# Performance work log

Measured on AMD Instinct MI355X. Metric: run time of the kernel, lower is better.

The kernel has to match this reference:

```python
import jax, jax.numpy as jnp
import numpy as np

K = 50          # NEC paper uses p=50 neighbors
DELTA = 1e-3    # kernel smoothing constant


def setup_inputs() -> dict:
    key = jax.random.key(0)
    ks = jax.random.split(key, 8)
    B, D_IN, D, A, C = 512, 2, 128, 3, 200000
    s = lambda fan_in: 1.0 / np.sqrt(fan_in)
    return {
        "x": jax.random.normal(ks[0], (B, D_IN), jnp.float32),
        "W1": jax.random.normal(ks[1], (D_IN, D), jnp.float32) * s(D_IN),
        "b1": jnp.zeros((D,), jnp.float32),
        "W2": jax.random.normal(ks[2], (D, D), jnp.float32) * s(D),
        "b2": jnp.zeros((D,), jnp.float32),
        "W3": jax.random.normal(ks[3], (D, D), jnp.float32) * s(D),
        "b3": jnp.zeros((D,), jnp.float32),
        "W4": jax.random.normal(ks[4], (D, D), jnp.float32) * s(D),
        "b4": jnp.zeros((D,), jnp.float32),
        "keys": jax.random.normal(ks[5], (A, C, D), jnp.float32),
        "mem_values": jax.random.normal(ks[6], (A, C), jnp.float32),
    }


def _encode(x, W1, b1, W2, b2, W3, b3, W4, b4):
    h = jax.nn.relu(x @ W1 + b1)
    h = jax.nn.relu(h @ W2 + b2)
    h = jax.nn.relu(h @ W3 + b3)
    return h @ W4 + b4  # [B, D]


def _dnd_lookup(h, keys, mem_values):
    # h: [B, D]; keys: [A, C, D]; mem_values: [A, C]
    q2 = jnp.sum(h * h, axis=-1)                       # [B]
    k2 = jnp.sum(keys * keys, axis=-1)                 # [A, C]
    cross = jnp.einsum("bd,acd->bac", h, keys)         # [B, A, C]
    d2 = jnp.maximum(q2[:, None, None] + k2[None] - 2.0 * cross, 0.0)
    neg_d, idx = jax.lax.top_k(-d2, K)                  # [B, A, K]
    d_top = -neg_d
    w = 1.0 / (d_top + DELTA)                           # NEC kernel
    w = w / jnp.sum(w, axis=-1, keepdims=True)
    a_idx = jnp.arange(keys.shape[0])[None, :, None]    # [1, A, 1]
    v_top = mem_values[a_idx, idx]                      # gather -> [B, A, K]
    values = jnp.sum(w * v_top, axis=-1)                # [B, A]
    return values


def reference(x, W1, b1, W2, b2, W3, b3, W4, b4, keys, mem_values):
    h = _encode(x, W1, b1, W2, b2, W3, b3, W4, b4)
    values = _dnd_lookup(h, keys, mem_values)
    actions = jnp.argmax(values, axis=-1)
    return values, actions
```

## Files before the change

kernel.cpp:

```cpp
#include <hip/hip_runtime.h>
#include <hip/hip_bf16.h>
#include <math.h>

#define B_    512
#define DIM   128
#define A_    3
#define C_    200000
#define K_    50
#define DELTA 1e-3

typedef __attribute__((ext_vector_type(8))) short bf16x8;
typedef __attribute__((ext_vector_type(4))) float f32x4;

#define NBIN_A 128
#define CAP_A  1024
#define NSEG_G 128
#define TPS_G  13
#define NT_G   1563
#define HSEG   16
#define CHPS   782
#define ROWCH  12500

#define AOFF_H64   0u
#define AOFF_H32   524288u
#define AOFF_HBF   786432u
#define AOFF_Q2    917504u
#define AOFF_HIST  919552u
#define AOFF_CNT   1705984u
#define AOFF_TAUB  1712128u
#define AOFF_V64   1718272u
#define AOFF_CAND  1730560u
#define AOFF_BINS  8022016u
#define NEED_A     (8022016ull + 307200000ull)

#define NBIN_B 192
#define CAP_B  768
#define BM_B   64
#define BN_B   128
#define TPC_B  16
#define CHUNK_B (TPC_B*BN_B)
#define NCH_B  ((C_ + CHUNK_B - 1)/CHUNK_B)

#define BOFF_H32   0u
#define BOFF_H64   262144u
#define BOFF_Q2    786432u
#define BOFF_K2    788480u
#define BOFF_HIST  3188480u
#define BOFF_TAU   4368128u
#define BOFF_CNT   4374272u
#define BOFF_V64   4380416u
#define BOFF_CAND  4392704u

static __device__ inline unsigned short f2bf(float x) {
    union { float f; unsigned u; } c; c.f = x;
    unsigned r = (c.u + 0x7FFFu + ((c.u >> 16) & 1u)) >> 16;
    return (unsigned short)r;
}
static __device__ inline unsigned pkbf(float a, float b) {
    __hip_bfloat162 t = __float22bfloat162_rn(make_float2(a, b));
    union { __hip_bfloat162 h; unsigned u; } cv; cv.h = t; return cv.u;
}

__global__ __launch_bounds__(128) void mlp_kernel(
    const float* __restrict__ x,
    const float* __restrict__ W1, const float* __restrict__ b1,
    const float* __restrict__ W2, const float* __restrict__ b2,
    const float* __restrict__ W3, const float* __restrict__ b3,
    const float* __restrict__ W4, const float* __restrict__ b4,
    float* __restrict__ h32, unsigned short* __restrict__ hbf,
    double* __restrict__ h64, float* __restrict__ q2)
{
    int b = blockIdx.x, t = threadIdx.x;
    __shared__ double s0[DIM], s1[DIM];
    double x0 = (double)x[b*2+0], x1 = (double)x[b*2+1];
    double h = x0*(double)W1[t] + x1*(double)W1[DIM+t] + (double)b1[t];
    s0[t] = h > 0.0 ? h : 0.0;
    __syncthreads();
    double acc = (double)b2[t];
    for (int k = 0; k < DIM; k++) acc += s0[k]*(double)W2[k*DIM+t];
    s1[t] = acc > 0.0 ? acc : 0.0;
    __syncthreads();
    acc = (double)b3[t];
    for (int k = 0; k < DIM; k++) acc += s1[k]*(double)W3[k*DIM+t];
    s0[t] = acc > 0.0 ? acc : 0.0;
    __syncthreads();
    acc = (double)b4[t];
    for (int k = 0; k < DIM; k++) acc += s0[k]*(double)W4[k*DIM+t];
    h64[b*DIM+t] = acc;
    float hf = (float)acc;
    h32[b*DIM+t] = hf;
    hbf[b*DIM+t] = f2bf(hf);
    s1[t] = acc*acc;
    __syncthreads();
    for (int s = 64; s > 0; s >>= 1) { if (t < s) s1[t] += s1[t+s]; __syncthreads(); }
    if (t == 0) q2[b] = (float)s1[0];
}

__global__ __launch_bounds__(512, 4) void gemm_bin_kernel(
    const float* __restrict__ keys, const unsigned short* __restrict__ hbf,
    const float* __restrict__ q2, unsigned char* __restrict__ bins)
{
    const int seg = blockIdx.x, my = blockIdx.y, a = blockIdx.z;
    const int b0 = my*128;
    const int tid = threadIdx.x;
    const int lane = tid & 63, w = tid >> 6;
    const int lm = lane & 15, kh = lane >> 4;
    const int wn = w & 3, wm = w >> 2;

    int tc = NT_G - seg*TPS_G;
    if (tc <= 0) return;
    if (tc > TPS_G) tc = TPS_G;

    __shared__ short sA[128*136];
    __shared__ short sB[128*136];
    __shared__ float q2s[128];
    __shared__ float k2s[128];

    const int r = tid >> 2, hh = tid & 3;

    {
        const int4* gp = (const int4*)hbf + (size_t)(b0 + r)*16 + hh*4;
        int4* dp = (int4*)&sA[r*136 + hh*32];
        #pragma unroll
        for (int q = 0; q < 4; q++) dp[q] = gp[q];
        if (tid < 128) q2s[tid] = q2[b0 + tid];
    }

    for (int t = 0; t < tc; t++) {
        int n0 = (seg*TPS_G + t)*128;
        __syncthreads();

        {
            int nr = n0 + r; if (nr >= C_) nr = C_-1;
            const float4* gp = (const float4*)(keys + ((size_t)a*C_ + nr)*128) + hh*8;
            float ss = 0.0f;
            int4* dp = (int4*)&sB[r*136 + hh*32];
            #pragma unroll
            for (int q = 0; q < 4; q++) {
                float4 v0 = gp[2*q], v1 = gp[2*q+1];
                ss += v0.x*v0.x + v0.y*v0.y + v0.z*v0.z + v0.w*v0.w
                    + v1.x*v1.x + v1.y*v1.y + v1.z*v1.z + v1.w*v1.w;
                int4 pk;
                pk.x = (int)pkbf(v0.x, v0.y);
                pk.y = (int)pkbf(v0.z, v0.w);
                pk.z = (int)pkbf(v1.x, v1.y);
                pk.w = (int)pkbf(v1.z, v1.w);
                dp[q] = pk;
            }
            ss += __shfl_xor(ss, 1, 64);
            ss += __shfl_xor(ss, 2, 64);
            if (hh == 0) k2s[r] = ss;
        }
        __syncthreads();

        f32x4 acc[2][4];
        #pragma unroll
        for (int i = 0; i < 2; i++)
            #pragma unroll
            for (int j = 0; j < 4; j++) acc[i][j] = (f32x4){0.f, 0.f, 0.f, 0.f};

        #pragma unroll
        for (int kst = 0; kst < 4; kst++) {
            bf16x8 af[2], bfv[4];
            #pragma unroll
            for (int i = 0; i < 2; i++)
                af[i] = *(const bf16x8*)&sB[(wn*32 + i*16 + lm)*136 + kst*32 + kh*8];
            #pragma unroll
            for (int j = 0; j < 4; j++)
                bfv[j] = *(const bf16x8*)&sA[(wm*64 + j*16 + lm)*136 + kst*32 + kh*8];
            #pragma unroll
            for (int i = 0; i < 2; i++)
                #pragma unroll
                for (int j = 0; j < 4; j++)
                    acc[i][j] = __builtin_amdgcn_mfma_f32_16x16x32_bf16(af[i], bfv[j], acc[i][j], 0, 0, 0);
        }

        unsigned char* bp = bins + ((size_t)(a*B_ + b0))*C_ + n0;
        #pragma unroll
        for (int i = 0; i < 2; i++) {
            int nl = wn*32 + i*16 + kh*4;
            int n = n0 + nl;
            if (n < C_) {
                float4 kq = *(const float4*)&k2s[nl];
                #pragma unroll
                for (int j = 0; j < 4; j++) {
                    int bcol = wm*64 + j*16 + lm;
                    float q2v = q2s[bcol];
                    unsigned pk = 0;
                    #pragma unroll
                    for (int rg = 0; rg < 4; rg++) {
                        float kv = (rg == 0) ? kq.x : (rg == 1) ? kq.y : (rg == 2) ? kq.z : kq.w;
                        float d2v = (q2v + kv) - 2.0f*acc[i][j][rg];
                        float dc = fminf(fmaxf(d2v, 16.0f), 4095.0f);
                        unsigned bin = (__float_as_uint(dc) >> 19) - 2096u;
                        pk |= bin << (8*rg);
                    }
                    *(unsigned*)(bp + (size_t)bcol*C_ + nl) = pk;
                }
            }
        }
    }
}

__global__ __launch_bounds__(256) void histA_kernel(const unsigned char* __restrict__ bins,
                                                    unsigned* __restrict__ hist)
{
    int q = blockIdx.x;
    int seg = blockIdx.y;
    int tid = threadIdx.x;
    int a = q >> 9, b = q & 511;
    int p = b*A_ + a;
    __shared__ unsigned hs[NBIN_A*8];
    for (int i = tid; i < NBIN_A*8; i += 256) hs[i] = 0;
    __syncthreads();
    const uint4* row = (const uint4*)(bins + (size_t)q*C_);
    int ch0 = seg*CHPS, ch1 = ch0 + CHPS; if (ch1 > ROWCH) ch1 = ROWCH;
    int rep = tid & 7;
    for (int ch = ch0 + tid; ch < ch1; ch += 256) {
        uint4 v = row[ch];
        unsigned d[4] = {v.x, v.y, v.z, v.w};
        #pragma unroll
        for (int e = 0; e < 4; e++) {
            unsigned x = d[e];
            atomicAdd(&hs[((x      ) & 127u)*8 + rep], 1u);
            atomicAdd(&hs[((x >>  8) & 127u)*8 + rep], 1u);
            atomicAdd(&hs[((x >> 16) & 127u)*8 + rep], 1u);
            atomicAdd(&hs[((x >> 24) & 127u)*8 + rep], 1u);
        }
    }
    __syncthreads();
    if (tid < NBIN_A) {
        unsigned s = 0;
        #pragma unroll
        for (int r2 = 0; r2 < 8; r2++) s += hs[tid*8 + r2];
        if (s) atomicAdd(&hist[(size_t)p*NBIN_A + tid], s);
    }
}

__global__ void tauA_kernel(const unsigned* __restrict__ hist, int* __restrict__ taubin)
{
    int p = blockIdx.x*256 + threadIdx.x;
    if (p >= B_*A_) return;
    const unsigned* hp = hist + (size_t)p*NBIN_A;
    unsigned cum = 0; int jsel = NBIN_A-1;
    for (int j = 0; j < NBIN_A; j++) { cum += hp[j]; if (cum >= K_) { jsel = j; break; } }
    unsigned c1 = cum + (jsel+1 < NBIN_A ? hp[jsel+1] : 0u);
    unsigned c2 = c1  + (jsel+2 < NBIN_A ? hp[jsel+2] : 0u);
    int jt = (c2 <= 768u) ? jsel+2 : jsel+1;
    if (jt > NBIN_A-1) jt = NBIN_A-1;
    taubin[p] = jt;
}

__global__ __launch_bounds__(256) void collectA_kernel(const unsigned char* __restrict__ bins,
    const int* __restrict__ taubin, unsigned* __restrict__ cnt, int* __restrict__ cand)
{
    int q = blockIdx.x, seg = blockIdx.y, tid = threadIdx.x;
    int a = q >> 9, b = q & 511;
    int p = b*A_ + a;
    int tb = taubin[p];
    unsigned thr  = (unsigned)(tb + 1);
    unsigned addv = (128u - thr) * 0x01010101u;
    const uint4* row = (const uint4*)(bins + (size_t)q*C_);
    int ch0 = seg*CHPS, ch1 = ch0 + CHPS; if (ch1 > ROWCH) ch1 = ROWCH;
    for (int ch = ch0 + tid; ch < ch1; ch += 256) {
        uint4 v = row[ch];
        unsigned d[4] = {v.x, v.y, v.z, v.w};
        #pragma unroll
        for (int e = 0; e < 4; e++) {
            unsigned m = (d[e] + addv) & 0x80808080u;
            if (m != 0x80808080u) {
                #pragma unroll
                for (int by = 0; by < 4; by++) {
                    if (!((m >> (8*by + 7)) & 1u)) {
                        int n = ch*16 + e*4 + by;
                        unsigned pos = atomicAdd(&cnt[p], 1u);
                        if (pos < CAP_A) cand[(size_t)p*CAP_A + pos] = n;
                    }
                }
            }
        }
    }
}

__global__ __launch_bounds__(256) void k2_kernel(const float* __restrict__ keys,
                                                 float* __restrict__ k2)
{
    int r = blockIdx.x*4 + (threadIdx.x >> 6);
    int lane = threadIdx.x & 63;
    float2 v = ((const float2*)keys)[(size_t)r*64 + lane];
    float s = v.x*v.x + v.y*v.y;
    #pragma unroll
    for (int off = 32; off > 0; off >>= 1) s += __shfl_down(s, off, 64);
    if (lane == 0) k2[r] = s;
}

template<int MODE>
__global__ __launch_bounds__(256) void pass_kernel(
    const float* __restrict__ keys, const float* __restrict__ h32,
    const float* __restrict__ q2,   const float* __restrict__ k2,
    unsigned* __restrict__ hist,    const float* __restrict__ tau,
    unsigned* __restrict__ cnt,     int* __restrict__ cand)
{
    const int bt = blockIdx.x;
    const int ch = blockIdx.y;
    const int a  = blockIdx.z;
    const int b0 = bt*BM_B;
    const int tid = threadIdx.x;
    const int tx = tid & 31, ty = tid >> 5;

    __shared__ float4 hs4[BM_B*33];
    __shared__ float4 ks4[BN_B*33];
    __shared__ float  q2s[BM_B];
    __shared__ float  taus[BM_B];
    __shared__ unsigned hist_s[MODE == 0 ? BM_B*NBIN_B : 1];

    #pragma unroll
    for (int q = 0; q < BM_B*32/256; q++) {
        int flat = q*256 + tid; int row = flat >> 5, kq = flat & 31;
        hs4[row*33 + kq] = ((const float4*)h32)[(size_t)(b0+row)*32 + kq];
    }
    if (tid < BM_B) {
        q2s[tid] = q2[b0+tid];
        if (MODE == 1) taus[tid] = tau[(b0+tid)*A_ + a];
    }
    if (MODE == 0) for (int i = tid; i < BM_B*NBIN_B; i += 256) hist_s[i] = 0;
    const float* __restrict__ k2g = k2 + (size_t)a*C_;

    for (int t = 0; t < TPC_B; t++) {
        int n0 = ch*CHUNK_B + t*BN_B;
        if (n0 >= C_) break;
        __syncthreads();
        #pragma unroll
        for (int q = 0; q < 16; q++) {
            int flat = q*256 + tid; int row = flat >> 5, kq = flat & 31;
            int nr = n0 + row; if (nr >= C_) nr = C_-1;
            ks4[row*33 + kq] = ((const float4*)keys)[((size_t)a*C_ + nr)*32 + kq];
        }
        __syncthreads();

        float acc[8][4];
        #pragma unroll
        for (int i = 0; i < 8; i++)
            #pragma unroll
            for (int j = 0; j < 4; j++) acc[i][j] = 0.0f;

        for (int kq = 0; kq < 32; kq++) {
            float4 hv[8], kv[4];
            #pragma unroll
            for (int i = 0; i < 8; i++) hv[i] = hs4[(ty*8+i)*33 + kq];
            #pragma unroll
            for (int j = 0; j < 4; j++) kv[j] = ks4[(j*32+tx)*33 + kq];
            #pragma unroll
            for (int i = 0; i < 8; i++)
                #pragma unroll
                for (int j = 0; j < 4; j++)
                    acc[i][j] += hv[i].x*kv[j].x + hv[i].y*kv[j].y
                               + hv[i].z*kv[j].z + hv[i].w*kv[j].w;
        }

        #pragma unroll
        for (int i = 0; i < 8; i++) {
            int bl = ty*8 + i;
            float q2b = q2s[bl];
            #pragma unroll
            for (int j = 0; j < 4; j++) {
                int n = n0 + j*32 + tx;
                if (n < C_) {
                    float d2f = fmaxf(q2b + k2g[n] - 2.0f*acc[i][j], 0.0f);
                    if (MODE == 0) {
                        int bin = (int)(__float_as_uint(d2f + 1.0f) >> 19) - 2032;
                        bin = bin < 0 ? 0 : (bin > NBIN_B-1 ? NBIN_B-1 : bin);
                        atomicAdd(&hist_s[bl*NBIN_B + bin], 1u);
                    } else {
                        if (d2f < taus[bl]) {
                            int p = (b0+bl)*A_ + a;
                            unsigned pos = atomicAdd(&cnt[p], 1u);
                            if (pos < CAP_B) cand[(size_t)p*CAP_B + pos] = n;
                        }
                    }
                }
            }
        }
    }
    if (MODE == 0) {
        __syncthreads();
        for (int i = tid; i < BM_B*NBIN_B; i += 256) {
            unsigned v = hist_s[i];
            if (v) {
                int bl = i / NBIN_B, bin = i % NBIN_B;
                atomicAdd(&hist[(size_t)((b0+bl)*A_ + a)*NBIN_B + bin], v);
            }
        }
    }
}

__global__ __launch_bounds__(256) void tauB_kernel(const unsigned* __restrict__ hist,
                                                   float* __restrict__ tau)
{
    int p = blockIdx.x*256 + threadIdx.x;
    if (p >= B_*A_) return;
    const unsigned* hp = hist + (size_t)p*NBIN_B;
    unsigned cum = 0; int jsel = NBIN_B-1;
    for (int j = 0; j < NBIN_B; j++) { cum += hp[j]; if (cum >= K_) { jsel = j; break; } }
    tau[p] = __uint_as_float((unsigned)(2034 + jsel) << 19) - 1.0f;
}

__global__ __launch_bounds__(256) void select_kernel(
    const float* __restrict__ keys, const double* __restrict__ h64,
    const float* __restrict__ mem_values,
    const unsigned* __restrict__ cnt, const int* __restrict__ cand,
    float* __restrict__ out_values, double* __restrict__ val64, int cap)
{
    int p = blockIdx.x; int b = p / A_, a = p % A_;
    int tid = threadIdx.x;
    __shared__ double hd[DIM];
    __shared__ double d2s[CAP_A];
    __shared__ float  vs[CAP_A];
    __shared__ double redv[4];
    __shared__ int    redi4[4];
    __shared__ double acc_w, acc_wv;

    for (int i = tid; i < DIM; i += 256) hd[i] = h64[(size_t)b*DIM + i];
    if (tid == 0) { acc_w = 0.0; acc_wv = 0.0; }
    __syncthreads();

    int n = (int)cnt[p]; if (n > cap) n = cap;
    for (int i = tid; i < n; i += 256) {
        int c = cand[(size_t)p*cap + i];
        const float4* kr = (const float4*)(keys + ((size_t)a*C_ + c)*DIM);
        double s0 = 0.0, s1 = 0.0;
        #pragma unroll 4
        for (int kq = 0; kq < 32; kq++) {
            float4 kv = kr[kq];
            double d0 = hd[4*kq+0] - (double)kv.x;
            double d1 = hd[4*kq+1] - (double)kv.y;
            double d2 = hd[4*kq+2] - (double)kv.z;
            double d3 = hd[4*kq+3] - (double)kv.w;
            s0 += d0*d0 + d1*d1; s1 += d2*d2 + d3*d3;
        }
        d2s[i] = s0 + s1;
        vs[i]  = mem_values[(size_t)a*C_ + c];
    }
    __syncthreads();

    int kk = n < K_ ? n : K_;
    for (int t = 0; t < kk; t++) {
        double best = 1e300; int bi = -1;
        for (int i = tid; i < n; i += 256)
            if (d2s[i] < best) { best = d2s[i]; bi = i; }
        #pragma unroll
        for (int off = 32; off > 0; off >>= 1) {
            double ov = __shfl_xor(best, off, 64);
            int    oi = __shfl_xor(bi,   off, 64);
            if (ov < best) { best = ov; bi = oi; }
        }
        int wv = tid >> 6;
        if ((tid & 63) == 0) { redv[wv] = best; redi4[wv] = bi; }
        __syncthreads();
        if (tid == 0) {
            double bv = redv[0]; int wi = redi4[0];
            if (redv[1] < bv) { bv = redv[1]; wi = redi4[1]; }
            if (redv[2] < bv) { bv = redv[2]; wi = redi4[2]; }
            if (redv[3] < bv) { bv = redv[3]; wi = redi4[3]; }
            double d = d2s[wi]; if (d < 0.0) d = 0.0;
            double wgt = 1.0 / (d + DELTA);
            acc_w += wgt; acc_wv += wgt * (double)vs[wi];
            d2s[wi] = 2e300;
        }
        __syncthreads();
    }
    if (tid == 0) {
        double v = acc_wv / acc_w;
        out_values[p] = (float)v;
        val64[p] = v;
    }
}

__global__ void argmax_kernel(const double* __restrict__ val64, float* __restrict__ out)
{
    int b = blockIdx.x*blockDim.x + threadIdx.x;
    if (b >= B_) return;
    double v0 = val64[b*A_+0], v1 = val64[b*A_+1], v2 = val64[b*A_+2];
    int bi = 0; double bv = v0;
    if (v1 > bv) { bv = v1; bi = 1; }
    if (v2 > bv) { bv = v2; bi = 2; }
    out[B_*A_ + b] = (float)bi;
}

extern "C" void kernel_launch(void* const* d_in, const int* in_sizes, int n_in,
                              void* d_out, int out_size, void* d_ws, size_t ws_size,
                              hipStream_t stream)
{
    const float* x    = (const float*)d_in[0];
    const float* W1   = (const float*)d_in[1];
    const float* b1   = (const float*)d_in[2];
    const float* W2   = (const float*)d_in[3];
    const float* b2   = (const float*)d_in[4];
    const float* W3   = (const float*)d_in[5];
    const float* b3   = (const float*)d_in[6];
    const float* W4   = (const float*)d_in[7];
    const float* b4   = (const float*)d_in[8];
    const float* keys = (const float*)d_in[9];
    const float* memv = (const float*)d_in[10];

    char* ws = (char*)d_ws;

    if (ws_size >= NEED_A) {
        double*         h64  = (double*)        (ws + AOFF_H64);
        float*          h32  = (float*)         (ws + AOFF_H32);
        unsigned short* hbf  = (unsigned short*)(ws + AOFF_HBF);
        float*          q2   = (float*)         (ws + AOFF_Q2);
        unsigned*       hist = (unsigned*)      (ws + AOFF_HIST);
        unsigned*       cnt  = (unsigned*)      (ws + AOFF_CNT);
        int*            taub = (int*)           (ws + AOFF_TAUB);
        double*         v64  = (double*)        (ws + AOFF_V64);
        int*            cand = (int*)           (ws + AOFF_CAND);
        unsigned char*  bins = (unsigned char*) (ws + AOFF_BINS);

        hipMemsetAsync(ws + AOFF_HIST, 0, (AOFF_CNT + B_*A_*4) - AOFF_HIST, stream);

        mlp_kernel<<<B_, 128, 0, stream>>>(x, W1, b1, W2, b2, W3, b3, W4, b4, h32, hbf, h64, q2);
        gemm_bin_kernel<<<dim3(NSEG_G, 4, A_), 512, 0, stream>>>(keys, hbf, q2, bins);
        histA_kernel<<<dim3(B_*A_, HSEG), 256, 0, stream>>>(bins, hist);
        tauA_kernel<<<(B_*A_ + 255)/256, 256, 0, stream>>>(hist, taub);
        collectA_kernel<<<dim3(B_*A_, HSEG), 256, 0, stream>>>(bins, taub, cnt, cand);
        select_kernel<<<B_*A_, 256, 0, stream>>>(keys, h64, memv, cnt, cand, (float*)d_out, v64, CAP_A);
        argmax_kernel<<<2, 256, 0, stream>>>(v64, (float*)d_out);
    } else {
        float*          h32  = (float*)         (ws + BOFF_H32);
        double*         h64  = (double*)        (ws + BOFF_H64);
        float*          q2   = (float*)         (ws + BOFF_Q2);
        float*          k2   = (float*)         (ws + BOFF_K2);
        unsigned*       hist = (unsigned*)      (ws + BOFF_HIST);
        float*          tau  = (float*)         (ws + BOFF_TAU);
        unsigned*       cnt  = (unsigned*)      (ws + BOFF_CNT);
        double*         v64  = (double*)        (ws + BOFF_V64);
        int*            cand = (int*)           (ws + BOFF_CAND);
        unsigned short* hbf  = (unsigned short*)(ws + BOFF_CAND);

        hipMemsetAsync(ws + BOFF_HIST, 0, (BOFF_CNT + B_*A_*4) - BOFF_HIST, stream);

        mlp_kernel<<<B_, 128, 0, stream>>>(x, W1, b1, W2, b2, W3, b3, W4, b4, h32, hbf, h64, q2);
        k2_kernel<<<(A_*C_)/4, 256, 0, stream>>>(keys, k2);
        pass_kernel<0><<<dim3(B_/BM_B, NCH_B, A_), 256, 0, stream>>>(keys, h32, q2, k2, hist, nullptr, nullptr, nullptr);
        tauB_kernel<<<(B_*A_ + 255)/256, 256, 0, stream>>>(hist, tau);
        pass_kernel<1><<<dim3(B_/BM_B, NCH_B, A_), 256, 0, stream>>>(keys, h32, q2, k2, nullptr, tau, cnt, cand);
        select_kernel<<<B_*A_, 256, 0, stream>>>(keys, h64, memv, cnt, cand, (float*)d_out, v64, CAP_B);
        argmax_kernel<<<2, 256, 0, stream>>>(v64, (float*)d_out);
    }
}
```

Baseline: 1.105 ms.

## Pre-convert keys to swizzled bf16 and double-buffer GEMM with direct-to-LDS loads

Adds a conversion pass that writes keys once as bf16 in an XOR-swizzled layout, together with precomputed key norms. A new GEMM kernel then streams these bf16 tiles into LDS with global_load_lds, double-buffered, instead of having each of the 4 row blocks re-read and re-convert the fp32 keys. The intent is to cut repeated fp32 key traffic and conversion work in the GEMM and to overlap loads with MFMA. The cost is an extra kernel with a full key read plus a bf16 write, a larger workspace requirement, and a path that falls back to the old kernel when the workspace is too small.

```diff
diff --git a/kernel.cpp b/kernel.cpp
--- a/kernel.cpp
+++ b/kernel.cpp
@@ -33,6 +33,14 @@
 #define AOFF_BINS  8022016u
 #define NEED_A     (8022016ull + 307200000ull)
 
+#define NSEG2  125
+#define TPS2   25
+#define NT2    3125
+#define KBF_ASTR 51200000ull
+#define AOFF_KBF 315222016ull
+#define AOFF_K2A (AOFF_KBF + 3ull*KBF_ASTR)
+#define NEED_A2  (AOFF_K2A + 2400000ull)
+
 #define NBIN_B 192
 #define CAP_B  768
 #define BM_B   64
@@ -61,6 +69,12 @@
     union { __hip_bfloat162 h; unsigned u; } cv; cv.h = t; return cv.u;
 }
 
+static __device__ inline void gl_lds16(const void* g, void* l) {
+    __builtin_amdgcn_global_load_lds(
+        (const __attribute__((address_space(1))) void*)g,
+        (__attribute__((address_space(3))) void*)l, 16, 0, 0);
+}
+
 __global__ __launch_bounds__(128) void mlp_kernel(
     const float* __restrict__ x,
     const float* __restrict__ W1, const float* __restrict__ b1,
@@ -96,6 +110,134 @@
     if (t == 0) q2[b] = (float)s1[0];
 }
 
+__global__ __launch_bounds__(256) void conv_kernel(
+    const float* __restrict__ keys, unsigned char* __restrict__ kbf,
+    float* __restrict__ k2a)
+{
+    int bid = blockIdx.x;
+    int a = bid / 12500;
+    int base = (bid - a*12500)*256 + threadIdx.x;
+    int n = base >> 4, cc = base & 15;
+    const float4* gp = (const float4*)(keys + ((size_t)a*C_ + n)*128 + cc*8);
+    float4 v0 = gp[0], v1 = gp[1];
+    float ss = v0.x*v0.x + v0.y*v0.y + v0.z*v0.z + v0.w*v0.w
+             + v1.x*v1.x + v1.y*v1.y + v1.z*v1.z + v1.w*v1.w;
+    int4 pk;
+    pk.x = (int)pkbf(v0.x, v0.y);
+    pk.y = (int)pkbf(v0.z, v0.w);
+    pk.z = (int)pkbf(v1.x, v1.y);
+    pk.w = (int)pkbf(v1.z, v1.w);
+    *(int4*)(kbf + (size_t)a*KBF_ASTR + (size_t)n*256 + ((cc ^ (n & 7)) << 4)) = pk;
+    ss += __shfl_xor(ss, 1, 64);
+    ss += __shfl_xor(ss, 2, 64);
+    ss += __shfl_xor(ss, 4, 64);
+    ss += __shfl_xor(ss, 8, 64);
+    if (cc == 0) k2a[(size_t)a*C_ + n] = ss;
+}
+
+__global__ __launch_bounds__(512, 4) void gemm2_kernel(
+    const unsigned char* __restrict__ kbf, const unsigned short* __restrict__ hbf,
+    const float* __restrict__ q2, const float* __restrict__ k2a,
+    unsigned char* __restrict__ bins)
+{
+    const int seg = blockIdx.x, my = blockIdx.y, a = blockIdx.z;
+    const int b0 = my*128;
+    const int tid = threadIdx.x;
+    const int lane = tid & 63, w = tid >> 6;
+    const int lm = lane & 15, kh = lane >> 4;
+    const int wn = w & 1, wm = w >> 1;
+
+    __shared__ short sA[16384];
+    __shared__ short sB[2][8192];
+    __shared__ float q2s[128];
+
+    {
+        int r = tid >> 2, hh = tid & 3;
+        const int4* gp = (const int4*)hbf + (size_t)(b0 + r)*16 + hh*4;
+        #pragma unroll
+        for (int q = 0; q < 4; q++) {
+            int cc = hh*4 + q;
+            *(int4*)((char*)sA + r*256 + ((cc ^ (r & 7)) << 4)) = gp[q];
+        }
+        if (tid < 128) q2s[tid] = q2[b0 + tid];
+    }
+
+    const unsigned char* kbfa = kbf + (size_t)a*KBF_ASTR;
+    const float* __restrict__ k2g = k2a + (size_t)a*C_;
+    const int t0 = seg*TPS2;
+
+    {
+        const char* src = (const char*)kbfa + (size_t)t0*16384 + tid*16;
+        char* dst = (char*)&sB[0][0] + w*1024;
+        gl_lds16(src, dst);
+        gl_lds16(src + 8192, dst + 8192);
+    }
+    __syncthreads();
+
+    int cur = 0;
+    for (int t = 0; t < TPS2; t++) {
+        int n0 = (t0 + t)*64;
+
+        if (t + 1 < TPS2) {
+            const char* src = (const char*)kbfa + (size_t)(t0 + t + 1)*16384 + tid*16;
+            char* dst = (char*)&sB[cur ^ 1][0] + w*1024;
+            gl_lds16(src, dst);
+            gl_lds16(src + 8192, dst + 8192);
+        }
+
+        f32x4 acc[2][2];
+        #pragma unroll
+        for (int i = 0; i < 2; i++)
+            #pragma unroll
+            for (int j = 0; j < 2; j++) acc[i][j] = (f32x4){0.f, 0.f, 0.f, 0.f};
+
+        const char* sBc = (const char*)&sB[cur][0];
+        #pragma unroll
+        for (int kst = 0; kst < 4; kst++) {
+            bf16x8 af[2], bfv[2];
+            #pragma unroll
+            for (int i = 0; i < 2; i++) {
+                int nr = wn*32 + i*16 + lm;
+                af[i] = *(const bf16x8*)(sBc + nr*256 + ((((kst<<2) + kh) ^ (nr & 7)) << 4));
+            }
+            #pragma unroll
+            for (int j = 0; j < 2; j++) {
+                int br = wm*32 + j*16 + lm;
+                bfv[j] = *(const bf16x8*)((const char*)sA + br*256 + ((((kst<<2) + kh) ^ (br & 7)) << 4));
+            }
+            #pragma unroll
+            for (int i = 0; i < 2; i++)
+                #pragma unroll
+                for (int j = 0; j < 2; j++)
+                    acc[i][j] = __builtin_amdgcn_mfma_f32_16x16x32_bf16(af[i], bfv[j], acc[i][j], 0, 0, 0);
+        }
+
+        unsigned char* bp = bins + ((size_t)(a*B_ + b0))*C_ + n0;
+        #pragma unroll
+        for (int i = 0; i < 2; i++) {
+            int nl = wn*32 + i*16 + kh*4;
+            float4 kq = *(const float4*)&k2g[n0 + nl];
+            #pragma unroll
+            for (int j = 0; j < 2; j++) {
+                int bcol = wm*32 + j*16 + lm;
+                float q2v = q2s[bcol];
+                unsigned pk = 0;
+                #pragma unroll
+                for (int rg = 0; rg < 4; rg++) {
+                    float kv = (rg == 0) ? kq.x : (rg == 1) ? kq.y : (rg == 2) ? kq.z : kq.w;
+                    float d2v = (q2v + kv) - 2.0f*acc[i][j][rg];
+                    float dc = fminf(fmaxf(d2v, 16.0f), 4095.0f);
+                    unsigned bin = (__float_as_uint(dc) >> 19) - 2096u;
+                    pk |= bin << (8*rg);
+                }
+                *(unsigned*)(bp + (size_t)bcol*C_ + nl) = pk;
+            }
+        }
+        __syncthreads();
+        cur ^= 1;
+    }
+}
+
 __global__ __launch_bounds__(512, 4) void gemm_bin_kernel(
     const float* __restrict__ keys, const unsigned short* __restrict__ hbf,
     const float* __restrict__ q2, unsigned char* __restrict__ bins)
@@ -112,12 +254,11 @@
     if (tc > TPS_G) tc = TPS_G;
 
     __shared__ short sA[128*136];
-    __shared__ short sB[128*136];
+    __shared__ short sB2[128*136];
     __shared__ float q2s[128];
     __shared__ float k2s[128];
 
     const int r = tid >> 2, hh = tid & 3;
-
     {
         const int4* gp = (const int4*)hbf + (size_t)(b0 + r)*16 + hh*4;
         int4* dp = (int4*)&sA[r*136 + hh*32];
@@ -129,12 +270,11 @@
     for (int t = 0; t < tc; t++) {
         int n0 = (seg*TPS_G + t)*128;
         __syncthreads();
-
         {
             int nr = n0 + r; if (nr >= C_) nr = C_-1;
             const float4* gp = (const float4*)(keys + ((size_t)a*C_ + nr)*128) + hh*8;
             float ss = 0.0f;
-            int4* dp = (int4*)&sB[r*136 + hh*32];
+            int4* dp = (int4*)&sB2[r*136 + hh*32];
             #pragma unroll
             for (int q = 0; q < 4; q++) {
                 float4 v0 = gp[2*q], v1 = gp[2*q+1];
@@ -164,7 +304,7 @@
             bf16x8 af[2], bfv[4];
             #pragma unroll
             for (int i = 0; i < 2; i++)
-                af[i] = *(const bf16x8*)&sB[(wn*32 + i*16 + lm)*136 + kst*32 + kh*8];
+                af[i] = *(const bf16x8*)&sB2[(wn*32 + i*16 + lm)*136 + kst*32 + kh*8];
             #pragma unroll
             for (int j = 0; j < 4; j++)
                 bfv[j] = *(const bf16x8*)&sA[(wm*64 + j*16 + lm)*136 + kst*32 + kh*8];
@@ -520,7 +660,16 @@
         hipMemsetAsync(ws + AOFF_HIST, 0, (AOFF_CNT + B_*A_*4) - AOFF_HIST, stream);
 
         mlp_kernel<<<B_, 128, 0, stream>>>(x, W1, b1, W2, b2, W3, b3, W4, b4, h32, hbf, h64, q2);
-        gemm_bin_kernel<<<dim3(NSEG_G, 4, A_), 512, 0, stream>>>(keys, hbf, q2, bins);
+
+        if (ws_size >= NEED_A2) {
+            unsigned char* kbf = (unsigned char*)(ws + AOFF_KBF);
+            float*         k2a = (float*)        (ws + AOFF_K2A);
+            conv_kernel<<<37500, 256, 0, stream>>>(keys, kbf, k2a);
+            gemm2_kernel<<<dim3(NSEG2, 4, A_), 512, 0, stream>>>(kbf, hbf, q2, k2a, bins);
+        } else {
+            gemm_bin_kernel<<<dim3(NSEG_G, 4, A_), 512, 0, stream>>>(keys, hbf, q2, bins);
+        }
+
         histA_kernel<<<dim3(B_*A_, HSEG), 256, 0, stream>>>(bins, hist);
         tauA_kernel<<<(B_*A_ + 255)/256, 256, 0, stream>>>(hist, taub);
         collectA_kernel<<<dim3(B_*A_, HSEG), 256, 0, stream>>>(bins, taub, cnt, cand);
```

New measurement: 1.145 ms. 1.04x slower.

## Double-buffer keys tile in GEMM and fuse histogram, threshold, collect, select per row

Applied to the files above, without the earlier changes.

Rewrites the GEMM-binning kernel to use 64-row key tiles with double-buffered, XOR-swizzled shared memory. It prefetches the next tile's global loads while MFMAs run on the current one. Histogram, threshold selection, candidate collection and exact top-K selection are merged into one per-(batch, action) block that keeps candidates in shared memory. This removes the memset, three kernel launches and the global hist/cand traffic. In exchange there is only one block per row instead of 16 segments, large shared-memory use per block, and a serial scan of the whole bins row per block.

```diff
diff --git a/kernel.cpp b/kernel.cpp
--- a/kernel.cpp
+++ b/kernel.cpp
@@ -14,22 +14,17 @@
 
 #define NBIN_A 128
 #define CAP_A  1024
-#define NSEG_G 128
-#define TPS_G  13
-#define NT_G   1563
-#define HSEG   16
-#define CHPS   782
 #define ROWCH  12500
+
+#define NSEG3  128
+#define TPS3   25
+#define NT3    3125
 
 #define AOFF_H64   0u
 #define AOFF_H32   524288u
 #define AOFF_HBF   786432u
 #define AOFF_Q2    917504u
-#define AOFF_HIST  919552u
-#define AOFF_CNT   1705984u
-#define AOFF_TAUB  1712128u
 #define AOFF_V64   1718272u
-#define AOFF_CAND  1730560u
 #define AOFF_BINS  8022016u
 #define NEED_A     (8022016ull + 307200000ull)
 
@@ -96,7 +91,40 @@
     if (t == 0) q2[b] = (float)s1[0];
 }
 
-__global__ __launch_bounds__(512, 4) void gemm_bin_kernel(
+static __device__ inline void load4(float4 lv[4], const float* __restrict__ ka,
+                                    int nrow, int hh) {
+    const float4* gp = (const float4*)(ka + (size_t)nrow*DIM) + hh*4;
+    #pragma unroll
+    for (int qq = 0; qq < 4; qq++) lv[qq] = gp[qq];
+}
+static __device__ inline void conv_store(const float4 lv[4], char* sBn,
+                                         float* k2n, int r, int hh) {
+    float ss = 0.f;
+    int4 pk0, pk1;
+    {
+        float4 v0 = lv[0], v1 = lv[1];
+        ss += v0.x*v0.x + v0.y*v0.y + v0.z*v0.z + v0.w*v0.w
+            + v1.x*v1.x + v1.y*v1.y + v1.z*v1.z + v1.w*v1.w;
+        pk0.x = (int)pkbf(v0.x, v0.y); pk0.y = (int)pkbf(v0.z, v0.w);
+        pk0.z = (int)pkbf(v1.x, v1.y); pk0.w = (int)pkbf(v1.z, v1.w);
+    }
+    {
+        float4 v0 = lv[2], v1 = lv[3];
+        ss += v0.x*v0.x + v0.y*v0.y + v0.z*v0.z + v0.w*v0.w
+            + v1.x*v1.x + v1.y*v1.y + v1.z*v1.z + v1.w*v1.w;
+        pk1.x = (int)pkbf(v0.x, v0.y); pk1.y = (int)pkbf(v0.z, v0.w);
+        pk1.z = (int)pkbf(v1.x, v1.y); pk1.w = (int)pkbf(v1.z, v1.w);
+    }
+    char* base = sBn + r*256;
+    *(int4*)(base + (((hh*2    ) ^ (r & 7)) << 4)) = pk0;
+    *(int4*)(base + (((hh*2 + 1) ^ (r & 7)) << 4)) = pk1;
+    ss += __shfl_xor(ss, 1, 64);
+    ss += __shfl_xor(ss, 2, 64);
+    ss += __shfl_xor(ss, 4, 64);
+    if (hh == 0) k2n[r] = ss;
+}
+
+__global__ __launch_bounds__(512, 2) void gemm3_kernel(
     const float* __restrict__ keys, const unsigned short* __restrict__ hbf,
     const float* __restrict__ q2, unsigned char* __restrict__ bins)
 {
@@ -105,73 +133,68 @@
     const int tid = threadIdx.x;
     const int lane = tid & 63, w = tid >> 6;
     const int lm = lane & 15, kh = lane >> 4;
-    const int wn = w & 3, wm = w >> 2;
-
-    int tc = NT_G - seg*TPS_G;
-    if (tc <= 0) return;
-    if (tc > TPS_G) tc = TPS_G;
-
-    __shared__ short sA[128*136];
-    __shared__ short sB[128*136];
+    const int wn = w & 1, wm = w >> 1;
+
+    const int tbeg = seg*TPS3;
+    int tcnt = NT3 - tbeg;
+    if (tcnt <= 0) return;
+    if (tcnt > TPS3) tcnt = TPS3;
+
+    __shared__ __align__(16) short sA[16384];
+    __shared__ __align__(16) short sB[2][8192];
     __shared__ float q2s[128];
-    __shared__ float k2s[128];
-
-    const int r = tid >> 2, hh = tid & 3;
+    __shared__ float k2s[2][64];
 
     {
-        const int4* gp = (const int4*)hbf + (size_t)(b0 + r)*16 + hh*4;
-        int4* dp = (int4*)&sA[r*136 + hh*32];
-        #pragma unroll
-        for (int q = 0; q < 4; q++) dp[q] = gp[q];
+        int r4 = tid >> 2, h4 = tid & 3;
+        const int4* gp = (const int4*)hbf + (size_t)(b0 + r4)*16 + h4*4;
+        #pragma unroll
+        for (int qq = 0; qq < 4; qq++) {
+            int cc = h4*4 + qq;
+            *(int4*)((char*)sA + r4*256 + ((cc ^ (r4 & 7)) << 4)) = gp[qq];
+        }
         if (tid < 128) q2s[tid] = q2[b0 + tid];
     }
 
-    for (int t = 0; t < tc; t++) {
-        int n0 = (seg*TPS_G + t)*128;
-        __syncthreads();
-
-        {
-            int nr = n0 + r; if (nr >= C_) nr = C_-1;
-            const float4* gp = (const float4*)(keys + ((size_t)a*C_ + nr)*128) + hh*8;
-            float ss = 0.0f;
-            int4* dp = (int4*)&sB[r*136 + hh*32];
-            #pragma unroll
-            for (int q = 0; q < 4; q++) {
-                float4 v0 = gp[2*q], v1 = gp[2*q+1];
-                ss += v0.x*v0.x + v0.y*v0.y + v0.z*v0.z + v0.w*v0.w
-                    + v1.x*v1.x + v1.y*v1.y + v1.z*v1.z + v1.w*v1.w;
-                int4 pk;
-                pk.x = (int)pkbf(v0.x, v0.y);
-                pk.y = (int)pkbf(v0.z, v0.w);
-                pk.z = (int)pkbf(v1.x, v1.y);
-                pk.w = (int)pkbf(v1.z, v1.w);
-                dp[q] = pk;
+    const int r = tid >> 3, hh = tid & 7;
+    const float* ka = keys + (size_t)a*C_*DIM;
+
+    float4 lv[4];
+    load4(lv, ka, tbeg*64 + r, hh);
+    conv_store(lv, (char*)&sB[0][0], k2s[0], r, hh);
+    __syncthreads();
+
+    int cur = 0;
+    for (int t = 0; t < tcnt; t++) {
+        const int n0 = (tbeg + t)*64;
+        const bool more = (t + 1 < tcnt);
+
+        if (more) load4(lv, ka, n0 + 64 + r, hh);
+
+        f32x4 acc[2][2];
+        #pragma unroll
+        for (int i = 0; i < 2; i++)
+            #pragma unroll
+            for (int j = 0; j < 2; j++) acc[i][j] = (f32x4){0.f, 0.f, 0.f, 0.f};
+
+        const char* sBc = (const char*)&sB[cur][0];
+        #pragma unroll
+        for (int kst = 0; kst < 4; kst++) {
+            bf16x8 af[2], bfv[2];
+            #pragma unroll
+            for (int i = 0; i < 2; i++) {
+                int nr = wn*32 + i*16 + lm;
+                af[i] = *(const bf16x8*)(sBc + nr*256 + ((((kst<<2) + kh) ^ (nr & 7)) << 4));
             }
-            ss += __shfl_xor(ss, 1, 64);
-            ss += __shfl_xor(ss, 2, 64);
-            if (hh == 0) k2s[r] = ss;
-        }
-        __syncthreads();
-
-        f32x4 acc[2][4];
-        #pragma unroll
-        for (int i = 0; i < 2; i++)
-            #pragma unroll
-            for (int j = 0; j < 4; j++) acc[i][j] = (f32x4){0.f, 0.f, 0.f, 0.f};
-
-        #pragma unroll
-        for (int kst = 0; kst < 4; kst++) {
-            bf16x8 af[2], bfv[4];
-            #pragma unroll
-            for (int i = 0; i < 2; i++)
-                af[i] = *(const bf16x8*)&sB[(wn*32 + i*16 + lm)*136 + kst*32 + kh*8];
-            #pragma unroll
-            for (int j = 0; j < 4; j++)
-                bfv[j] = *(const bf16x8*)&sA[(wm*64 + j*16 + lm)*136 + kst*32 + kh*8];
+            #pragma unroll
+            for (int j = 0; j < 2; j++) {
+                int br = wm*32 + j*16 + lm;
+                bfv[j] = *(const bf16x8*)((const char*)sA + br*256 + ((((kst<<2) + kh) ^ (br & 7)) << 4));
+            }
             #pragma unroll
             for (int i = 0; i < 2; i++)
                 #pragma unroll
-                for (int j = 0; j < 4; j++)
+                for (int j = 0; j < 2; j++)
                     acc[i][j] = __builtin_amdgcn_mfma_f32_16x16x32_bf16(af[i], bfv[j], acc[i][j], 0, 0, 0);
         }
 
@@ -179,90 +202,92 @@
         #pragma unroll
         for (int i = 0; i < 2; i++) {
             int nl = wn*32 + i*16 + kh*4;
-            int n = n0 + nl;
-            if (n < C_) {
-                float4 kq = *(const float4*)&k2s[nl];
+            float4 kq = *(const float4*)&k2s[cur][nl];
+            #pragma unroll
+            for (int j = 0; j < 2; j++) {
+                int bcol = wm*32 + j*16 + lm;
+                float q2v = q2s[bcol];
+                unsigned pk = 0;
                 #pragma unroll
-                for (int j = 0; j < 4; j++) {
-                    int bcol = wm*64 + j*16 + lm;
-                    float q2v = q2s[bcol];
-                    unsigned pk = 0;
-                    #pragma unroll
-                    for (int rg = 0; rg < 4; rg++) {
-                        float kv = (rg == 0) ? kq.x : (rg == 1) ? kq.y : (rg == 2) ? kq.z : kq.w;
-                        float d2v = (q2v + kv) - 2.0f*acc[i][j][rg];
-                        float dc = fminf(fmaxf(d2v, 16.0f), 4095.0f);
-                        unsigned bin = (__float_as_uint(dc) >> 19) - 2096u;
-                        pk |= bin << (8*rg);
-                    }
-                    *(unsigned*)(bp + (size_t)bcol*C_ + nl) = pk;
+                for (int rg = 0; rg < 4; rg++) {
+                    float kv = (rg == 0) ? kq.x : (rg == 1) ? kq.y : (rg == 2) ? kq.z : kq.w;
+                    float d2v = (q2v + kv) - 2.0f*acc[i][j][rg];
+                    float dc = fminf(fmaxf(d2v, 16.0f), 4095.0f);
+                    unsigned bin = (__float_as_uint(dc) >> 19) - 2096u;
+                    pk |= bin << (8*rg);
                 }
+                *(unsigned*)(bp + (size_t)bcol*C_ + nl) = pk;
             }
         }
-    }
-}
-
-__global__ __launch_bounds__(256) void histA_kernel(const unsigned char* __restrict__ bins,
-                                                    unsigned* __restrict__ hist)
-{
-    int q = blockIdx.x;
-    int seg = blockIdx.y;
-    int tid = threadIdx.x;
-    int a = q >> 9, b = q & 511;
-    int p = b*A_ + a;
-    __shared__ unsigned hs[NBIN_A*8];
-    for (int i = tid; i < NBIN_A*8; i += 256) hs[i] = 0;
-    __syncthreads();
+
+        if (more) conv_store(lv, (char*)&sB[cur ^ 1][0], k2s[cur ^ 1], r, hh);
+        __syncthreads();
+        cur ^= 1;
+    }
+}
+
+__global__ __launch_bounds__(256) void finish_kernel(
+    const unsigned char* __restrict__ bins, const float* __restrict__ keys,
+    const double* __restrict__ h64, const float* __restrict__ mem_values,
+    float* __restrict__ out_values, double* __restrict__ val64)
+{
+    const int q = blockIdx.x;
+    const int a = q >> 9, b = q & 511;
+    const int p = b*A_ + a;
+    const int tid = threadIdx.x;
+
+    __shared__ unsigned hist_s[NBIN_A*8];
+    __shared__ unsigned hc[NBIN_A];
+    __shared__ double hd[DIM];
+    __shared__ int    cidx[CAP_A];
+    __shared__ double d2s[CAP_A];
+    __shared__ float  vs[CAP_A];
+    __shared__ double redv[4];
+    __shared__ int    redi4[4];
+    __shared__ double acc_w, acc_wv;
+    __shared__ unsigned cnt_s;
+    __shared__ int thr_s;
+
+    for (int i = tid; i < NBIN_A*8; i += 256) hist_s[i] = 0;
+    for (int i = tid; i < DIM; i += 256) hd[i] = h64[(size_t)b*DIM + i];
+    if (tid == 0) { cnt_s = 0; acc_w = 0.0; acc_wv = 0.0; }
+    __syncthreads();
+
     const uint4* row = (const uint4*)(bins + (size_t)q*C_);
-    int ch0 = seg*CHPS, ch1 = ch0 + CHPS; if (ch1 > ROWCH) ch1 = ROWCH;
-    int rep = tid & 7;
-    for (int ch = ch0 + tid; ch < ch1; ch += 256) {
+    const int rep = tid & 7;
+    for (int ch = tid; ch < ROWCH; ch += 256) {
         uint4 v = row[ch];
         unsigned d[4] = {v.x, v.y, v.z, v.w};
         #pragma unroll
         for (int e = 0; e < 4; e++) {
             unsigned x = d[e];
-            atomicAdd(&hs[((x      ) & 127u)*8 + rep], 1u);
-            atomicAdd(&hs[((x >>  8) & 127u)*8 + rep], 1u);
-            atomicAdd(&hs[((x >> 16) & 127u)*8 + rep], 1u);
-            atomicAdd(&hs[((x >> 24) & 127u)*8 + rep], 1u);
+            atomicAdd(&hist_s[((x      ) & 127u)*8 + rep], 1u);
+            atomicAdd(&hist_s[((x >>  8) & 127u)*8 + rep], 1u);
+            atomicAdd(&hist_s[((x >> 16) & 127u)*8 + rep], 1u);
+            atomicAdd(&hist_s[((x >> 24) & 127u)*8 + rep], 1u);
         }
     }
     __syncthreads();
     if (tid < NBIN_A) {
         unsigned s = 0;
         #pragma unroll
-        for (int r2 = 0; r2 < 8; r2++) s += hs[tid*8 + r2];
-        if (s) atomicAdd(&hist[(size_t)p*NBIN_A + tid], s);
-    }
-}
-
-__global__ void tauA_kernel(const unsigned* __restrict__ hist, int* __restrict__ taubin)
-{
-    int p = blockIdx.x*256 + threadIdx.x;
-    if (p >= B_*A_) return;
-    const unsigned* hp = hist + (size_t)p*NBIN_A;
-    unsigned cum = 0; int jsel = NBIN_A-1;
-    for (int j = 0; j < NBIN_A; j++) { cum += hp[j]; if (cum >= K_) { jsel = j; break; } }
-    unsigned c1 = cum + (jsel+1 < NBIN_A ? hp[jsel+1] : 0u);
-    unsigned c2 = c1  + (jsel+2 < NBIN_A ? hp[jsel+2] : 0u);
-    int jt = (c2 <= 768u) ? jsel+2 : jsel+1;
-    if (jt > NBIN_A-1) jt = NBIN_A-1;
-    taubin[p] = jt;
-}
-
-__global__ __launch_bounds__(256) void collectA_kernel(const unsigned char* __restrict__ bins,
-    const int* __restrict__ taubin, unsigned* __restrict__ cnt, int* __restrict__ cand)
-{
-    int q = blockIdx.x, seg = blockIdx.y, tid = threadIdx.x;
-    int a = q >> 9, b = q & 511;
-    int p = b*A_ + a;
-    int tb = taubin[p];
-    unsigned thr  = (unsigned)(tb + 1);
-    unsigned addv = (128u - thr) * 0x01010101u;
-    const uint4* row = (const uint4*)(bins + (size_t)q*C_);
-    int ch0 = seg*CHPS, ch1 = ch0 + CHPS; if (ch1 > ROWCH) ch1 = ROWCH;
-    for (int ch = ch0 + tid; ch < ch1; ch += 256) {
+        for (int r2 = 0; r2 < 8; r2++) s += hist_s[tid*8 + r2];
+        hc[tid] = s;
+    }
+    __syncthreads();
+    if (tid == 0) {
+        unsigned cum = 0; int jsel = NBIN_A-1;
+        for (int j = 0; j < NBIN_A; j++) { cum += hc[j]; if (cum >= K_) { jsel = j; break; } }
+        unsigned c1 = cum + (jsel+1 < NBIN_A ? hc[jsel+1] : 0u);
+        unsigned c2 = c1  + (jsel+2 < NBIN_A ? hc[jsel+2] : 0u);
+        int jt = (c2 <= 768u) ? jsel+2 : jsel+1;
+        if (jt > NBIN_A-1) jt = NBIN_A-1;
+        thr_s = jt + 1;
+    }
+    __syncthreads();
+    const unsigned thr  = (unsigned)thr_s;
+    const unsigned addv = (128u - thr) * 0x01010101u;
+    for (int ch = tid; ch < ROWCH; ch += 256) {
         uint4 v = row[ch];
         unsigned d[4] = {v.x, v.y, v.z, v.w};
         #pragma unroll
@@ -272,13 +297,64 @@
                 #pragma unroll
                 for (int by = 0; by < 4; by++) {
                     if (!((m >> (8*by + 7)) & 1u)) {
-                        int n = ch*16 + e*4 + by;
-                        unsigned pos = atomicAdd(&cnt[p], 1u);
-                        if (pos < CAP_A) cand[(size_t)p*CAP_A + pos] = n;
+                        unsigned pos = atomicAdd(&cnt_s, 1u);
+                        if (pos < CAP_A) cidx[pos] = ch*16 + e*4 + by;
                     }
                 }
             }
         }
+    }
+    __syncthreads();
+    int n = (int)cnt_s; if (n > CAP_A) n = CAP_A;
+
+    for (int i = tid; i < n; i += 256) {
+        int c = cidx[i];
+        const float4* kr = (const float4*)(keys + ((size_t)a*C_ + c)*DIM);
+        double s0 = 0.0, s1 = 0.0;
+        #pragma unroll 4
+        for (int kq = 0; kq < 32; kq++) {
+            float4 kv = kr[kq];
+            double d0 = hd[4*kq+0] - (double)kv.x;
+            double d1 = hd[4*kq+1] - (double)kv.y;
+            double d2 = hd[4*kq+2] - (double)kv.z;
+            double d3 = hd[4*kq+3] - (double)kv.w;
+            s0 += d0*d0 + d1*d1; s1 += d2*d2 + d3*d3;
+        }
+        d2s[i] = s0 + s1;
+        vs[i]  = mem_values[(size_t)a*C_ + c];
+    }
+    __syncthreads();
+
+    int kk = n < K_ ? n : K_;
+    for (int t = 0; t < kk; t++) {
+        double best = 1e300; int bi = -1;
+        for (int i = tid; i < n; i += 256)
+            if (d2s[i] < best) { best = d2s[i]; bi = i; }
+        #pragma unroll
+        for (int off = 32; off > 0; off >>= 1) {
+            double ov = __shfl_xor(best, off, 64);
+            int    oi = __shfl_xor(bi,   off, 64);
+            if (ov < best) { best = ov; bi = oi; }
+        }
+        int wv = tid >> 6;
+        if ((tid & 63) == 0) { redv[wv] = best; redi4[wv] = bi; }
+        __syncthreads();
+        if (tid == 0) {
+            double bv = redv[0]; int wi = redi4[0];
+            if (redv[1] < bv) { bv = redv[1]; wi = redi4[1]; }
+            if (redv[2] < bv) { bv = redv[2]; wi = redi4[2]; }
+            if (redv[3] < bv) { bv = redv[3]; wi = redi4[3]; }
+            double d = d2s[wi]; if (d < 0.0) d = 0.0;
+            double wgt = 1.0 / (d + DELTA);
+            acc_w += wgt; acc_wv += wgt * (double)vs[wi];
+            d2s[wi] = 2e300;
+        }
+        __syncthreads();
+    }
+    if (tid == 0) {
+        double v = acc_wv / acc_w;
+        out_values[p] = (float)v;
+        val64[p] = v;
     }
 }
 
@@ -510,21 +586,12 @@
         float*          h32  = (float*)         (ws + AOFF_H32);
         unsigned short* hbf  = (unsigned short*)(ws + AOFF_HBF);
         float*          q2   = (float*)         (ws + AOFF_Q2);
-        unsigned*       hist = (unsigned*)      (ws + AOFF_HIST);
-        unsigned*       cnt  = (unsigned*)      (ws + AOFF_CNT);
-        int*            taub = (int*)           (ws + AOFF_TAUB);
         double*         v64  = (double*)        (ws + AOFF_V64);
-        int*            cand = (int*)           (ws + AOFF_CAND);
         unsigned char*  bins = (unsigned char*) (ws + AOFF_BINS);
 
-        hipMemsetAsync(ws + AOFF_HIST, 0, (AOFF_CNT + B_*A_*4) - AOFF_HIST, stream);
-
         mlp_kernel<<<B_, 128, 0, stream>>>(x, W1, b1, W2, b2, W3, b3, W4, b4, h32, hbf, h64, q2);
-        gemm_bin_kernel<<<dim3(NSEG_G, 4, A_), 512, 0, stream>>>(keys, hbf, q2, bins);
-        histA_kernel<<<dim3(B_*A_, HSEG), 256, 0, stream>>>(bins, hist);
-        tauA_kernel<<<(B_*A_ + 255)/256, 256, 0, stream>>>(hist, taub);
-        collectA_kernel<<<dim3(B_*A_, HSEG), 256, 0, stream>>>(bins, taub, cnt, cand);
-        select_kernel<<<B_*A_, 256, 0, stream>>>(keys, h64, memv, cnt, cand, (float*)d_out, v64, CAP_A);
+        gemm3_kernel<<<dim3(NSEG3, 4, A_), 512, 0, stream>>>(keys, hbf, q2, bins);
+        finish_kernel<<<B_*A_, 256, 0, stream>>>(bins, keys, h64, memv, (float*)d_out, v64);
         argmax_kernel<<<2, 256, 0, stream>>>(v64, (float*)d_out);
     } else {
         float*          h32  = (float*)         (ws + BOFF_H32);
```

Result: faster. 960.1 us (-13.1%).
